# Performance work log

Measured on AMD Instinct MI355X. Metric: run time of the kernel, lower is better.

Reference implementation:

```python
import jax, jax.numpy as jnp
import numpy as np

# Mamba hyperparams (mamba_ssm defaults for d_model=128)
D_MODEL = 128
DEPTH = 8
D_INNER = 256   # expand=2
D_STATE = 16
D_CONV = 4
DT_RANK = 8     # ceil(D_MODEL/16)
EPS = 1e-5


def setup_inputs() -> dict:
    key = jax.random.key(0)
    ks = jax.random.split(key, 8)
    B, H, W = 1, 48, 48
    s = lambda k, shape, sc=0.02: jax.random.normal(k, shape, jnp.float32) * sc
    return {
        "x": jax.random.normal(ks[0], (B, D_MODEL, H, W), jnp.float32),
        "W_in": s(ks[1], (DEPTH, D_MODEL, 2 * D_INNER)),
        "conv_w": s(ks[2], (DEPTH, D_INNER, D_CONV), 0.2),
        "conv_b": jnp.zeros((DEPTH, D_INNER), jnp.float32),
        "W_xproj": s(ks[3], (DEPTH, D_INNER, DT_RANK + 2 * D_STATE)),
        "W_dt": s(ks[4], (DEPTH, DT_RANK, D_INNER), 0.1),
        "b_dt": jnp.full((DEPTH, D_INNER), -4.6, jnp.float32),  # softplus ~= 0.01
        "A_log": jnp.broadcast_to(
            jnp.log(jnp.arange(1, D_STATE + 1, dtype=jnp.float32)),
            (DEPTH, D_INNER, D_STATE)).copy(),
        "D_skip": jnp.ones((DEPTH, D_INNER), jnp.float32),
        "W_out": s(ks[5], (DEPTH, D_INNER, D_MODEL)),
        "rms_w": jnp.ones((DEPTH, D_MODEL), jnp.float32),
    }


def _rmsnorm(x, w):
    return x * jax.lax.rsqrt(jnp.mean(x * x, axis=-1, keepdims=True) + EPS) * w


def _mamba_layer(x, Wi, cw, cb, Wx, Wdt, bdt, Alog, Dp, Wo):
    # x: [B, L, D_MODEL]
    B, L, _ = x.shape
    xz = x @ Wi                                   # [B, L, 2*d_inner]
    xi, z = jnp.split(xz, 2, axis=-1)
    # causal depthwise conv1d, kernel D_CONV
    xp = jnp.pad(xi, ((0, 0), (D_CONV - 1, 0), (0, 0)))
    xc = sum(xp[:, k:k + L, :] * cw[:, k] for k in range(D_CONV)) + cb
    xc = jax.nn.silu(xc)                          # [B, L, d_inner]
    dbl = xc @ Wx                                 # [B, L, dt_rank + 2*d_state]
    dt_r = dbl[..., :DT_RANK]
    Bs = dbl[..., DT_RANK:DT_RANK + D_STATE]      # [B, L, d_state]
    Cs = dbl[..., DT_RANK + D_STATE:]
    dt = jax.nn.softplus(dt_r @ Wdt + bdt)        # [B, L, d_inner]
    A = -jnp.exp(Alog)                            # [d_inner, d_state]
    dA = jnp.exp(dt[..., None] * A)               # [B, L, d_inner, d_state]
    dBx = (dt * xc)[..., None] * Bs[:, :, None, :]
    # linear recurrence h_t = dA_t * h_{t-1} + dBx_t via parallel scan
    def comb(l, r):
        al, bl = l
        ar, br = r
        return ar * al, ar * bl + br
    _, h = jax.lax.associative_scan(comb, (dA, dBx), axis=1)
    y = jnp.einsum('blds,bls->bld', h, Cs) + Dp * xc
    y = y * jax.nn.silu(z)
    return y @ Wo                                 # [B, L, D_MODEL]


def reference(x, W_in, conv_w, conv_b, W_xproj, W_dt, b_dt, A_log, D_skip, W_out, rms_w):
    B, C, H, W = x.shape
    seq = x.reshape(B, C, H * W).transpose(0, 2, 1)  # [B, L, C]
    for l in range(DEPTH):
        seq = _mamba_layer(seq, W_in[l], conv_w[l], conv_b[l], W_xproj[l],
                           W_dt[l], b_dt[l], A_log[l], D_skip[l], W_out[l])
        seq = _rmsnorm(seq, rms_w[l])
    return seq.reshape(B, H, W, C).transpose(0, 3, 1, 2)
```

## Files before the change

kernel.cpp:

```cpp
#include <hip/hip_runtime.h>
#include <math.h>

#define LSEQ 2304
#define DM 128
#define DI 256
#define DS 16
#define RK 8
#define NCH 576
#define CLEN 4
#define NG 24
#define GS 24
#define NSI (DI*DS)
#define EPSF 1e-5f

__device__ __forceinline__ float silu_f(float s) { return s / (1.f + __expf(-s)); }
__device__ __forceinline__ float softplus_f(float x) { return (x > 20.f) ? x : log1pf(__expf(x)); }

template<bool FIRST>
__global__ __launch_bounds__(256, 4)
void k_in(const float* __restrict__ seq, const float* __restrict__ x0,
          const float* __restrict__ Wi,
          const float* __restrict__ cw, const float* __restrict__ cbias,
          float* __restrict__ xc_g, float* __restrict__ sz_g) {
    __shared__ float As[19 * 128];
    const int l0 = blockIdx.x * 16;
    const int half = blockIdx.y & 1;
    const bool isZ = blockIdx.y >= 2;
    const int tid = threadIdx.x;

    if (FIRST) {
        const int rlo = isZ ? 3 : 0;
        for (int idx = tid + rlo * 128; idx < 19 * 128; idx += 256) {
            const int r = idx >> 7, cc = idx & 127;
            const int l = l0 - 3 + r;
            As[idx] = (l >= 0) ? x0[cc * LSEQ + l] : 0.f;
        }
    } else if (!isZ) {
        for (int idx = tid; idx < 19 * 32; idx += 256) {
            const int r = idx >> 5, cq = (idx & 31) * 4;
            const int l = l0 - 3 + r;
            const float4 v = (l >= 0) ? *(const float4*)&seq[l * DM + cq]
                                      : make_float4(0.f, 0.f, 0.f, 0.f);
            *(float4*)&As[r * 128 + cq] = v;
        }
    } else {
        for (int idx = tid; idx < 16 * 32; idx += 256) {
            const int r = 3 + (idx >> 5), cq = (idx & 31) * 4;
            *(float4*)&As[r * 128 + cq] =
                *(const float4*)&seq[(l0 - 3 + r) * DM + cq];
        }
    }
    __syncthreads();

    const int c = tid & 127;
    const int rg = tid >> 7;
    const int d = half * 128 + c;

    if (!isZ) {
        float ax[11];
#pragma unroll
        for (int r = 0; r < 11; ++r) ax[r] = 0.f;
        for (int k4 = 0; k4 < 32; ++k4) {
            float bv[4];
#pragma unroll
            for (int u = 0; u < 4; ++u) bv[u] = Wi[(k4 * 4 + u) * 512 + d];
#pragma unroll
            for (int r = 0; r < 11; ++r) {
                const float4 a4 = *(const float4*)&As[(rg * 8 + r) * 128 + k4 * 4];
                ax[r] += a4.x * bv[0] + a4.y * bv[1] + a4.z * bv[2] + a4.w * bv[3];
            }
        }
        const float w0 = cw[d * 4 + 0], w1 = cw[d * 4 + 1];
        const float w2 = cw[d * 4 + 2], w3 = cw[d * 4 + 3];
        const float cbv = cbias[d];
#pragma unroll
        for (int rr = 0; rr < 8; ++rr) {
            const float v = silu_f(cbv + w0 * ax[rr] + w1 * ax[rr + 1] +
                                   w2 * ax[rr + 2] + w3 * ax[rr + 3]);
            xc_g[(l0 + rg * 8 + rr) * DI + d] = v;
        }
    } else {
        float az[8];
#pragma unroll
        for (int r = 0; r < 8; ++r) az[r] = 0.f;
        for (int k4 = 0; k4 < 32; ++k4) {
            float bv[4];
#pragma unroll
            for (int u = 0; u < 4; ++u) bv[u] = Wi[(k4 * 4 + u) * 512 + 256 + d];
#pragma unroll
            for (int r = 0; r < 8; ++r) {
                const float4 a4 = *(const float4*)&As[(rg * 8 + r + 3) * 128 + k4 * 4];
                az[r] += a4.x * bv[0] + a4.y * bv[1] + a4.z * bv[2] + a4.w * bv[3];
            }
        }
#pragma unroll
        for (int rr = 0; rr < 8; ++rr)
            sz_g[(l0 + rg * 8 + rr) * DI + d] = silu_f(az[rr]);
    }
}

__global__ __launch_bounds__(256, 4)
void k_mid2(const float* __restrict__ xc_g,
            const float* __restrict__ Wx,
            const float* __restrict__ Wdt, const float* __restrict__ bdt,
            const float* __restrict__ Alog,
            float* __restrict__ dbl_g, float* __restrict__ dt_g,
            float* __restrict__ P, float* __restrict__ S) {
    __shared__ float xcs[CLEN * 256];
    __shared__ float part[4 * 160];
    __shared__ float dtrs[CLEN * 8];
    __shared__ float dbls[CLEN * 32];
    const int c = blockIdx.x;
    const int l0 = c * CLEN;
    const int tid = threadIdx.x;
    const int d = tid;

    ((float4*)xcs)[tid] = ((const float4*)&xc_g[l0 * DI])[tid];
    __syncthreads();

    for (int task = tid; task < 640; task += 256) {
        const int kc = task / 160;
        const int o = task - kc * 160;
        const int r = o / 40, j = o - r * 40;
        const float* xr = &xcs[r * 256 + kc * 64];
        const float* wp = &Wx[(kc * 64) * 40 + j];
        float acc = 0.f;
#pragma unroll 8
        for (int k = 0; k < 64; ++k) acc += xr[k] * wp[k * 40];
        part[kc * 160 + o] = acc;
    }
    __syncthreads();
    if (tid < 160) {
        const float acc = part[tid] + part[160 + tid] + part[320 + tid] + part[480 + tid];
        const int r = tid / 40, j = tid - r * 40;
        if (j < RK) dtrs[r * 8 + j] = acc;
        else {
            dbls[r * 32 + (j - 8)] = acc;
            dbl_g[(l0 + r) * 32 + (j - 8)] = acc;
        }
    }
    __syncthreads();

    float dtv[CLEN], xcv[CLEN];
    {
        float wdt[8];
#pragma unroll
        for (int q = 0; q < 8; ++q) wdt[q] = Wdt[q * DI + d];
        const float bdv = bdt[d];
#pragma unroll
        for (int r = 0; r < CLEN; ++r) {
            float acc = bdv;
#pragma unroll
            for (int q = 0; q < 8; ++q) acc += dtrs[r * 8 + q] * wdt[q];
            dtv[r] = softplus_f(acc);
            dt_g[(l0 + r) * DI + d] = dtv[r];
            xcv[r] = xcs[r * 256 + d];
        }
    }

    float A[16], pr[16], hs[16];
#pragma unroll
    for (int v = 0; v < 4; ++v) {
        const float4 a4 = *(const float4*)&Alog[d * DS + v * 4];
        A[v * 4 + 0] = -__expf(a4.x);
        A[v * 4 + 1] = -__expf(a4.y);
        A[v * 4 + 2] = -__expf(a4.z);
        A[v * 4 + 3] = -__expf(a4.w);
    }
#pragma unroll
    for (int s = 0; s < 16; ++s) { pr[s] = 1.f; hs[s] = 0.f; }
#pragma unroll
    for (int t = 0; t < CLEN; ++t) {
        const float dtt = dtv[t];
        const float uv = dtt * xcv[t];
        const float* Brow = &dbls[t * 32];
#pragma unroll
        for (int s = 0; s < 16; ++s) {
            const float e = __expf(dtt * A[s]);
            pr[s] *= e;
            hs[s] = e * hs[s] + uv * Brow[s];
        }
    }
    const int base = c * NSI + d * DS;
#pragma unroll
    for (int v = 0; v < 4; ++v) {
        *(float4*)&P[base + v * 4] =
            make_float4(pr[v * 4], pr[v * 4 + 1], pr[v * 4 + 2], pr[v * 4 + 3]);
        *(float4*)&S[base + v * 4] =
            make_float4(hs[v * 4], hs[v * 4 + 1], hs[v * 4 + 2], hs[v * 4 + 3]);
    }
}

__global__ __launch_bounds__(256, 4)
void k_carry1(float* __restrict__ P, float* __restrict__ S,
              float* __restrict__ Pg, float* __restrict__ Sg) {
    const int g = blockIdx.x;
    const int i = blockIdx.y * 256 + threadIdx.x;
    float G = 0.f, Pp = 1.f;
    const int base = g * GS * NSI + i;
#pragma unroll 8
    for (int k = 0; k < GS; ++k) {
        const int idx = base + k * NSI;
        const float p = P[idx];
        const float s = S[idx];
        S[idx] = G;
        P[idx] = Pp;
        G = p * G + s;
        Pp *= p;
    }
    Pg[g * NSI + i] = Pp;
    Sg[g * NSI + i] = G;
}

__global__ __launch_bounds__(256, 4)
void k_carry2(const float* __restrict__ Pg, float* __restrict__ Sg) {
    const int i = blockIdx.x * 256 + threadIdx.x;
    float G = 0.f;
#pragma unroll 8
    for (int g = 0; g < NG; ++g) {
        const int idx = g * NSI + i;
        const float p = Pg[idx];
        const float s = Sg[idx];
        Sg[idx] = G;
        G = p * G + s;
    }
}

template<bool LAST>
__global__ __launch_bounds__(256, 3)
void k_tail(const float* __restrict__ dt_g, const float* __restrict__ xc_g,
            const float* __restrict__ dbl_g, const float* __restrict__ Alog,
            const float* __restrict__ Sloc, const float* __restrict__ Ppre,
            const float* __restrict__ Gc, const float* __restrict__ Dp,
            const float* __restrict__ sz_g, const float* __restrict__ Wo,
            const float* __restrict__ rmsw, float* __restrict__ seq,
            float* __restrict__ out) {
    __shared__ float dbls[CLEN * 32];
    __shared__ float Ys[CLEN * 256];
    __shared__ float partO[4 * CLEN * 128];
    __shared__ float Os[CLEN * 129];
    __shared__ float red[CLEN * 32];
    __shared__ float scaleS[CLEN];
    const int c = blockIdx.x;
    const int g = c / GS;
    const int l0 = c * CLEN;
    const int tid = threadIdx.x;
    const int d = tid;

    if (tid < CLEN * 32) dbls[tid] = dbl_g[l0 * 32 + tid];

    float A[16], h[16];
#pragma unroll
    for (int v = 0; v < 4; ++v) {
        const float4 a4 = *(const float4*)&Alog[d * DS + v * 4];
        A[v * 4 + 0] = -__expf(a4.x);
        A[v * 4 + 1] = -__expf(a4.y);
        A[v * 4 + 2] = -__expf(a4.z);
        A[v * 4 + 3] = -__expf(a4.w);
        const float4 s4 = *(const float4*)&Sloc[c * NSI + d * DS + v * 4];
        const float4 p4 = *(const float4*)&Ppre[c * NSI + d * DS + v * 4];
        const float4 g4 = *(const float4*)&Gc[g * NSI + d * DS + v * 4];
        h[v * 4 + 0] = s4.x + p4.x * g4.x;
        h[v * 4 + 1] = s4.y + p4.y * g4.y;
        h[v * 4 + 2] = s4.z + p4.z * g4.z;
        h[v * 4 + 3] = s4.w + p4.w * g4.w;
    }
    float dtv[CLEN], xcv[CLEN], szv[CLEN];
#pragma unroll
    for (int r = 0; r < CLEN; ++r) {
        dtv[r] = dt_g[(l0 + r) * DI + d];
        xcv[r] = xc_g[(l0 + r) * DI + d];
        szv[r] = sz_g[(l0 + r) * DI + d];
    }
    const float dskip = Dp[d];
    __syncthreads();
#pragma unroll
    for (int t = 0; t < CLEN; ++t) {
        const float dtt = dtv[t];
        const float uv = dtt * xcv[t];
        float sum = 0.f;
#pragma unroll
        for (int s = 0; s < 16; ++s) {
            const float e = __expf(dtt * A[s]);
            h[s] = e * h[s] + uv * dbls[t * 32 + s];
            sum += h[s] * dbls[t * 32 + 16 + s];
        }
        Ys[t * 256 + d] = (sum + dskip * xcv[t]) * szv[t];
    }
    __syncthreads();

    {
        const int ccp = tid & 63;
        const int kg = tid >> 6;
        float acc[CLEN][2];
#pragma unroll
        for (int r = 0; r < CLEN; ++r) { acc[r][0] = 0.f; acc[r][1] = 0.f; }
        const float* wp = &Wo[(kg * 64) * DM + ccp * 2];
        const float* yp = &Ys[kg * 64];
#pragma unroll 4
        for (int k4 = 0; k4 < 16; ++k4) {
            const float2 w0 = *(const float2*)(wp + (k4 * 4 + 0) * DM);
            const float2 w1 = *(const float2*)(wp + (k4 * 4 + 1) * DM);
            const float2 w2 = *(const float2*)(wp + (k4 * 4 + 2) * DM);
            const float2 w3 = *(const float2*)(wp + (k4 * 4 + 3) * DM);
            float4 y4[CLEN];
#pragma unroll
            for (int r = 0; r < CLEN; ++r)
                y4[r] = *(const float4*)&yp[r * 256 + k4 * 4];
#pragma unroll
            for (int r = 0; r < CLEN; ++r) {
                acc[r][0] += y4[r].x * w0.x; acc[r][1] += y4[r].x * w0.y;
            }
#pragma unroll
            for (int r = 0; r < CLEN; ++r) {
                acc[r][0] += y4[r].y * w1.x; acc[r][1] += y4[r].y * w1.y;
            }
#pragma unroll
            for (int r = 0; r < CLEN; ++r) {
                acc[r][0] += y4[r].z * w2.x; acc[r][1] += y4[r].z * w2.y;
            }
#pragma unroll
            for (int r = 0; r < CLEN; ++r) {
                acc[r][0] += y4[r].w * w3.x; acc[r][1] += y4[r].w * w3.y;
            }
        }
#pragma unroll
        for (int r = 0; r < CLEN; ++r) {
            partO[(kg * CLEN + r) * 128 + ccp * 2 + 0] = acc[r][0];
            partO[(kg * CLEN + r) * 128 + ccp * 2 + 1] = acc[r][1];
        }
        __syncthreads();
        for (int idx = tid; idx < CLEN * 128; idx += 256) {
            const int r = idx >> 7, cc = idx & 127;
            Os[r * 129 + cc] = partO[(0 * CLEN + r) * 128 + cc] +
                               partO[(1 * CLEN + r) * 128 + cc] +
                               partO[(2 * CLEN + r) * 128 + cc] +
                               partO[(3 * CLEN + r) * 128 + cc];
        }
        __syncthreads();
    }

    if (tid < CLEN * 32) {
        const int r = tid >> 5, part = tid & 31;
        float ss = 0.f;
#pragma unroll
        for (int i = 0; i < 4; ++i) {
            const float v = Os[r * 129 + part * 4 + i];
            ss += v * v;
        }
        red[tid] = ss;
    }
    __syncthreads();
    if (tid < CLEN) {
        float ss = 0.f;
#pragma unroll
        for (int p = 0; p < 32; ++p) ss += red[tid * 32 + p];
        scaleS[tid] = rsqrtf(ss * (1.f / DM) + EPSF);
    }
    __syncthreads();
    if (LAST) {
        for (int idx = tid; idx < CLEN * DM; idx += 256) {
            const int r = idx >> 7, cc = idx & 127;
            out[cc * LSEQ + (l0 + r)] = Os[r * 129 + cc] * scaleS[r] * rmsw[cc];
        }
    } else {
        for (int idx = tid; idx < CLEN * DM; idx += 256) {
            const int r = idx >> 7, cc = idx & 127;
            seq[(l0 + r) * DM + cc] = Os[r * 129 + cc] * scaleS[r] * rmsw[cc];
        }
    }
}

extern "C" void kernel_launch(void* const* d_in, const int* in_sizes, int n_in,
                              void* d_out, int out_size, void* d_ws, size_t ws_size,
                              hipStream_t stream) {
    const float* x    = (const float*)d_in[0];
    const float* W_in = (const float*)d_in[1];
    const float* cw   = (const float*)d_in[2];
    const float* cb   = (const float*)d_in[3];
    const float* Wx   = (const float*)d_in[4];
    const float* Wdt  = (const float*)d_in[5];
    const float* bdt  = (const float*)d_in[6];
    const float* Alog = (const float*)d_in[7];
    const float* Dp   = (const float*)d_in[8];
    const float* Wo   = (const float*)d_in[9];
    const float* rmsw = (const float*)d_in[10];
    float* out = (float*)d_out;

    float* ws   = (float*)d_ws;
    float* seq  = ws; ws += LSEQ * DM;
    float* szb  = ws; ws += LSEQ * DI;
    float* xcb  = ws; ws += LSEQ * DI;
    float* dtb  = ws; ws += LSEQ * DI;
    float* dblb = ws; ws += LSEQ * 32;
    float* Pb   = ws; ws += NCH * NSI;
    float* Sb   = ws; ws += NCH * NSI;
    float* Pgb  = ws; ws += NG * NSI;
    float* Sgb  = ws; ws += NG * NSI;

    for (int layer = 0; layer < 8; ++layer) {
        const float* Wi_l   = W_in + (size_t)layer * DM * 512;
        const float* cw_l   = cw   + (size_t)layer * DI * 4;
        const float* cb_l   = cb   + (size_t)layer * DI;
        const float* Wx_l   = Wx   + (size_t)layer * DI * 40;
        const float* Wdt_l  = Wdt  + (size_t)layer * RK * DI;
        const float* bdt_l  = bdt  + (size_t)layer * DI;
        const float* Alog_l = Alog + (size_t)layer * DI * DS;
        const float* Dp_l   = Dp   + (size_t)layer * DI;
        const float* Wo_l   = Wo   + (size_t)layer * DI * DM;
        const float* rmsw_l = rmsw + (size_t)layer * DM;

        if (layer == 0)
            k_in<true><<<dim3(144, 4), 256, 0, stream>>>(seq, x, Wi_l, cw_l, cb_l,
                                                         xcb, szb);
        else
            k_in<false><<<dim3(144, 4), 256, 0, stream>>>(seq, x, Wi_l, cw_l, cb_l,
                                                          xcb, szb);

        k_mid2<<<NCH, 256, 0, stream>>>(xcb, Wx_l, Wdt_l, bdt_l, Alog_l,
                                        dblb, dtb, Pb, Sb);

        k_carry1<<<dim3(NG, 16), 256, 0, stream>>>(Pb, Sb, Pgb, Sgb);
        k_carry2<<<16, 256, 0, stream>>>(Pgb, Sgb);

        if (layer == 7)
            k_tail<true><<<NCH, 256, 0, stream>>>(dtb, xcb, dblb, Alog_l, Sb, Pb,
                                                  Sgb, Dp_l, szb, Wo_l, rmsw_l,
                                                  seq, out);
        else
            k_tail<false><<<NCH, 256, 0, stream>>>(dtb, xcb, dblb, Alog_l, Sb, Pb,
                                                   Sgb, Dp_l, szb, Wo_l, rmsw_l,
                                                   seq, out);
    }
}
```

Before: 556.7 us.

## Double threads per block in k_in, k_mid2 and k_tail, splitting state dimension

```diff
diff --git a/kernel.cpp b/kernel.cpp
--- a/kernel.cpp
+++ b/kernel.cpp
@@ -17,7 +17,7 @@
 __device__ __forceinline__ float softplus_f(float x) { return (x > 20.f) ? x : log1pf(__expf(x)); }
 
 template<bool FIRST>
-__global__ __launch_bounds__(256, 4)
+__global__ __launch_bounds__(512, 4)
 void k_in(const float* __restrict__ seq, const float* __restrict__ x0,
           const float* __restrict__ Wi,
           const float* __restrict__ cw, const float* __restrict__ cbias,
@@ -30,13 +30,13 @@
 
     if (FIRST) {
         const int rlo = isZ ? 3 : 0;
-        for (int idx = tid + rlo * 128; idx < 19 * 128; idx += 256) {
+        for (int idx = tid + rlo * 128; idx < 19 * 128; idx += 512) {
             const int r = idx >> 7, cc = idx & 127;
             const int l = l0 - 3 + r;
             As[idx] = (l >= 0) ? x0[cc * LSEQ + l] : 0.f;
         }
     } else if (!isZ) {
-        for (int idx = tid; idx < 19 * 32; idx += 256) {
+        for (int idx = tid; idx < 19 * 32; idx += 512) {
             const int r = idx >> 5, cq = (idx & 31) * 4;
             const int l = l0 - 3 + r;
             const float4 v = (l >= 0) ? *(const float4*)&seq[l * DM + cq]
@@ -44,7 +44,7 @@
             *(float4*)&As[r * 128 + cq] = v;
         }
     } else {
-        for (int idx = tid; idx < 16 * 32; idx += 256) {
+        for (int idx = tid; idx < 16 * 32; idx += 512) {
             const int r = 3 + (idx >> 5), cq = (idx & 31) * 4;
             *(float4*)&As[r * 128 + cq] =
                 *(const float4*)&seq[(l0 - 3 + r) * DM + cq];
@@ -57,16 +57,16 @@
     const int d = half * 128 + c;
 
     if (!isZ) {
-        float ax[11];
-#pragma unroll
-        for (int r = 0; r < 11; ++r) ax[r] = 0.f;
+        float ax[7];
+#pragma unroll
+        for (int r = 0; r < 7; ++r) ax[r] = 0.f;
         for (int k4 = 0; k4 < 32; ++k4) {
             float bv[4];
 #pragma unroll
             for (int u = 0; u < 4; ++u) bv[u] = Wi[(k4 * 4 + u) * 512 + d];
 #pragma unroll
-            for (int r = 0; r < 11; ++r) {
-                const float4 a4 = *(const float4*)&As[(rg * 8 + r) * 128 + k4 * 4];
+            for (int r = 0; r < 7; ++r) {
+                const float4 a4 = *(const float4*)&As[(rg * 4 + r) * 128 + k4 * 4];
                 ax[r] += a4.x * bv[0] + a4.y * bv[1] + a4.z * bv[2] + a4.w * bv[3];
             }
         }
@@ -74,32 +74,32 @@
         const float w2 = cw[d * 4 + 2], w3 = cw[d * 4 + 3];
         const float cbv = cbias[d];
 #pragma unroll
-        for (int rr = 0; rr < 8; ++rr) {
+        for (int rr = 0; rr < 4; ++rr) {
             const float v = silu_f(cbv + w0 * ax[rr] + w1 * ax[rr + 1] +
                                    w2 * ax[rr + 2] + w3 * ax[rr + 3]);
-            xc_g[(l0 + rg * 8 + rr) * DI + d] = v;
+            xc_g[(l0 + rg * 4 + rr) * DI + d] = v;
         }
     } else {
-        float az[8];
-#pragma unroll
-        for (int r = 0; r < 8; ++r) az[r] = 0.f;
+        float az[4];
+#pragma unroll
+        for (int r = 0; r < 4; ++r) az[r] = 0.f;
         for (int k4 = 0; k4 < 32; ++k4) {
             float bv[4];
 #pragma unroll
             for (int u = 0; u < 4; ++u) bv[u] = Wi[(k4 * 4 + u) * 512 + 256 + d];
 #pragma unroll
-            for (int r = 0; r < 8; ++r) {
-                const float4 a4 = *(const float4*)&As[(rg * 8 + r + 3) * 128 + k4 * 4];
+            for (int r = 0; r < 4; ++r) {
+                const float4 a4 = *(const float4*)&As[(rg * 4 + r + 3) * 128 + k4 * 4];
                 az[r] += a4.x * bv[0] + a4.y * bv[1] + a4.z * bv[2] + a4.w * bv[3];
             }
         }
 #pragma unroll
-        for (int rr = 0; rr < 8; ++rr)
-            sz_g[(l0 + rg * 8 + rr) * DI + d] = silu_f(az[rr]);
-    }
-}
-
-__global__ __launch_bounds__(256, 4)
+        for (int rr = 0; rr < 4; ++rr)
+            sz_g[(l0 + rg * 4 + rr) * DI + d] = silu_f(az[rr]);
+    }
+}
+
+__global__ __launch_bounds__(512, 4)
 void k_mid2(const float* __restrict__ xc_g,
             const float* __restrict__ Wx,
             const float* __restrict__ Wdt, const float* __restrict__ bdt,
@@ -113,12 +113,13 @@
     const int c = blockIdx.x;
     const int l0 = c * CLEN;
     const int tid = threadIdx.x;
-    const int d = tid;
-
-    ((float4*)xcs)[tid] = ((const float4*)&xc_g[l0 * DI])[tid];
-    __syncthreads();
-
-    for (int task = tid; task < 640; task += 256) {
+    const int d = tid >> 1;
+    const int sh = tid & 1;
+
+    if (tid < 256) ((float4*)xcs)[tid] = ((const float4*)&xc_g[l0 * DI])[tid];
+    __syncthreads();
+
+    for (int task = tid; task < 640; task += 512) {
         const int kc = task / 160;
         const int o = task - kc * 160;
         const int r = o / 40, j = o - r * 40;
@@ -153,37 +154,37 @@
 #pragma unroll
             for (int q = 0; q < 8; ++q) acc += dtrs[r * 8 + q] * wdt[q];
             dtv[r] = softplus_f(acc);
-            dt_g[(l0 + r) * DI + d] = dtv[r];
+            if (sh == 0) dt_g[(l0 + r) * DI + d] = dtv[r];
             xcv[r] = xcs[r * 256 + d];
         }
     }
 
-    float A[16], pr[16], hs[16];
-#pragma unroll
-    for (int v = 0; v < 4; ++v) {
-        const float4 a4 = *(const float4*)&Alog[d * DS + v * 4];
+    float A[8], pr[8], hs[8];
+#pragma unroll
+    for (int v = 0; v < 2; ++v) {
+        const float4 a4 = *(const float4*)&Alog[tid * 8 + v * 4];
         A[v * 4 + 0] = -__expf(a4.x);
         A[v * 4 + 1] = -__expf(a4.y);
         A[v * 4 + 2] = -__expf(a4.z);
         A[v * 4 + 3] = -__expf(a4.w);
     }
 #pragma unroll
-    for (int s = 0; s < 16; ++s) { pr[s] = 1.f; hs[s] = 0.f; }
+    for (int s = 0; s < 8; ++s) { pr[s] = 1.f; hs[s] = 0.f; }
 #pragma unroll
     for (int t = 0; t < CLEN; ++t) {
         const float dtt = dtv[t];
         const float uv = dtt * xcv[t];
-        const float* Brow = &dbls[t * 32];
-#pragma unroll
-        for (int s = 0; s < 16; ++s) {
+        const float* Brow = &dbls[t * 32 + sh * 8];
+#pragma unroll
+        for (int s = 0; s < 8; ++s) {
             const float e = __expf(dtt * A[s]);
             pr[s] *= e;
             hs[s] = e * hs[s] + uv * Brow[s];
         }
     }
-    const int base = c * NSI + d * DS;
-#pragma unroll
-    for (int v = 0; v < 4; ++v) {
+    const int base = c * NSI + tid * 8;
+#pragma unroll
+    for (int v = 0; v < 2; ++v) {
         *(float4*)&P[base + v * 4] =
             make_float4(pr[v * 4], pr[v * 4 + 1], pr[v * 4 + 2], pr[v * 4 + 3]);
         *(float4*)&S[base + v * 4] =
@@ -227,7 +228,7 @@
 }
 
 template<bool LAST>
-__global__ __launch_bounds__(256, 3)
+__global__ __launch_bounds__(512, 4)
 void k_tail(const float* __restrict__ dt_g, const float* __restrict__ xc_g,
             const float* __restrict__ dbl_g, const float* __restrict__ Alog,
             const float* __restrict__ Sloc, const float* __restrict__ Ppre,
@@ -237,7 +238,7 @@
             float* __restrict__ out) {
     __shared__ float dbls[CLEN * 32];
     __shared__ float Ys[CLEN * 256];
-    __shared__ float partO[4 * CLEN * 128];
+    __shared__ float partO[8 * CLEN * 128];
     __shared__ float Os[CLEN * 129];
     __shared__ float red[CLEN * 32];
     __shared__ float scaleS[CLEN];
@@ -245,21 +246,22 @@
     const int g = c / GS;
     const int l0 = c * CLEN;
     const int tid = threadIdx.x;
-    const int d = tid;
+    const int d = tid >> 1;
+    const int sh = tid & 1;
 
     if (tid < CLEN * 32) dbls[tid] = dbl_g[l0 * 32 + tid];
 
-    float A[16], h[16];
-#pragma unroll
-    for (int v = 0; v < 4; ++v) {
-        const float4 a4 = *(const float4*)&Alog[d * DS + v * 4];
+    float A[8], h[8];
+#pragma unroll
+    for (int v = 0; v < 2; ++v) {
+        const float4 a4 = *(const float4*)&Alog[tid * 8 + v * 4];
         A[v * 4 + 0] = -__expf(a4.x);
         A[v * 4 + 1] = -__expf(a4.y);
         A[v * 4 + 2] = -__expf(a4.z);
         A[v * 4 + 3] = -__expf(a4.w);
-        const float4 s4 = *(const float4*)&Sloc[c * NSI + d * DS + v * 4];
-        const float4 p4 = *(const float4*)&Ppre[c * NSI + d * DS + v * 4];
-        const float4 g4 = *(const float4*)&Gc[g * NSI + d * DS + v * 4];
+        const float4 s4 = *(const float4*)&Sloc[c * NSI + tid * 8 + v * 4];
+        const float4 p4 = *(const float4*)&Ppre[c * NSI + tid * 8 + v * 4];
+        const float4 g4 = *(const float4*)&Gc[g * NSI + tid * 8 + v * 4];
         h[v * 4 + 0] = s4.x + p4.x * g4.x;
         h[v * 4 + 1] = s4.y + p4.y * g4.y;
         h[v * 4 + 2] = s4.z + p4.z * g4.z;
@@ -278,14 +280,17 @@
     for (int t = 0; t < CLEN; ++t) {
         const float dtt = dtv[t];
         const float uv = dtt * xcv[t];
-        float sum = 0.f;
-#pragma unroll
-        for (int s = 0; s < 16; ++s) {
+        const float* Brow = &dbls[t * 32 + sh * 8];
+        const float* Crow = &dbls[t * 32 + 16 + sh * 8];
+        float ps = 0.f;
+#pragma unroll
+        for (int s = 0; s < 8; ++s) {
             const float e = __expf(dtt * A[s]);
-            h[s] = e * h[s] + uv * dbls[t * 32 + s];
-            sum += h[s] * dbls[t * 32 + 16 + s];
-        }
-        Ys[t * 256 + d] = (sum + dskip * xcv[t]) * szv[t];
+            h[s] = e * h[s] + uv * Brow[s];
+            ps += h[s] * Crow[s];
+        }
+        ps += __shfl_xor(ps, 1);
+        if (sh == 0) Ys[t * 256 + d] = (ps + dskip * xcv[t]) * szv[t];
     }
     __syncthreads();
 
@@ -295,10 +300,10 @@
         float acc[CLEN][2];
 #pragma unroll
         for (int r = 0; r < CLEN; ++r) { acc[r][0] = 0.f; acc[r][1] = 0.f; }
-        const float* wp = &Wo[(kg * 64) * DM + ccp * 2];
-        const float* yp = &Ys[kg * 64];
+        const float* wp = &Wo[(kg * 32) * DM + ccp * 2];
+        const float* yp = &Ys[kg * 32];
 #pragma unroll 4
-        for (int k4 = 0; k4 < 16; ++k4) {
+        for (int k4 = 0; k4 < 8; ++k4) {
             const float2 w0 = *(const float2*)(wp + (k4 * 4 + 0) * DM);
             const float2 w1 = *(const float2*)(wp + (k4 * 4 + 1) * DM);
             const float2 w2 = *(const float2*)(wp + (k4 * 4 + 2) * DM);
@@ -330,22 +335,23 @@
             partO[(kg * CLEN + r) * 128 + ccp * 2 + 1] = acc[r][1];
         }
         __syncthreads();
-        for (int idx = tid; idx < CLEN * 128; idx += 256) {
+        for (int idx = tid; idx < CLEN * 128; idx += 512) {
             const int r = idx >> 7, cc = idx & 127;
-            Os[r * 129 + cc] = partO[(0 * CLEN + r) * 128 + cc] +
-                               partO[(1 * CLEN + r) * 128 + cc] +
-                               partO[(2 * CLEN + r) * 128 + cc] +
-                               partO[(3 * CLEN + r) * 128 + cc];
+            float s = 0.f;
+#pragma unroll
+            for (int kgi = 0; kgi < 8; ++kgi)
+                s += partO[(kgi * CLEN + r) * 128 + cc];
+            Os[r * 129 + cc] = s;
         }
         __syncthreads();
     }
 
     if (tid < CLEN * 32) {
-        const int r = tid >> 5, part = tid & 31;
+        const int r = tid >> 5, pp = tid & 31;
         float ss = 0.f;
 #pragma unroll
         for (int i = 0; i < 4; ++i) {
-            const float v = Os[r * 129 + part * 4 + i];
+            const float v = Os[r * 129 + pp * 4 + i];
             ss += v * v;
         }
         red[tid] = ss;
@@ -359,12 +365,12 @@
     }
     __syncthreads();
     if (LAST) {
-        for (int idx = tid; idx < CLEN * DM; idx += 256) {
+        for (int idx = tid; idx < CLEN * DM; idx += 512) {
             const int r = idx >> 7, cc = idx & 127;
             out[cc * LSEQ + (l0 + r)] = Os[r * 129 + cc] * scaleS[r] * rmsw[cc];
         }
     } else {
-        for (int idx = tid; idx < CLEN * DM; idx += 256) {
+        for (int idx = tid; idx < CLEN * DM; idx += 512) {
             const int r = idx >> 7, cc = idx & 127;
             seq[(l0 + r) * DM + cc] = Os[r * 129 + cc] * scaleS[r] * rmsw[cc];
         }
@@ -411,24 +417,24 @@
         const float* rmsw_l = rmsw + (size_t)layer * DM;
 
         if (layer == 0)
-            k_in<true><<<dim3(144, 4), 256, 0, stream>>>(seq, x, Wi_l, cw_l, cb_l,
+            k_in<true><<<dim3(144, 4), 512, 0, stream>>>(seq, x, Wi_l, cw_l, cb_l,
                                                          xcb, szb);
         else
-            k_in<false><<<dim3(144, 4), 256, 0, stream>>>(seq, x, Wi_l, cw_l, cb_l,
+            k_in<false><<<dim3(144, 4), 512, 0, stream>>>(seq, x, Wi_l, cw_l, cb_l,
                                                           xcb, szb);
 
-        k_mid2<<<NCH, 256, 0, stream>>>(xcb, Wx_l, Wdt_l, bdt_l, Alog_l,
+        k_mid2<<<NCH, 512, 0, stream>>>(xcb, Wx_l, Wdt_l, bdt_l, Alog_l,
                                         dblb, dtb, Pb, Sb);
 
         k_carry1<<<dim3(NG, 16), 256, 0, stream>>>(Pb, Sb, Pgb, Sgb);
         k_carry2<<<16, 256, 0, stream>>>(Pgb, Sgb);
 
         if (layer == 7)
-            k_tail<true><<<NCH, 256, 0, stream>>>(dtb, xcb, dblb, Alog_l, Sb, Pb,
+            k_tail<true><<<NCH, 512, 0, stream>>>(dtb, xcb, dblb, Alog_l, Sb, Pb,
                                                   Sgb, Dp_l, szb, Wo_l, rmsw_l,
                                                   seq, out);
         else
-            k_tail<false><<<NCH, 256, 0, stream>>>(dtb, xcb, dblb, Alog_l, Sb, Pb,
+            k_tail<false><<<NCH, 512, 0, stream>>>(dtb, xcb, dblb, Alog_l, Sb, Pb,
                                                    Sgb, Dp_l, szb, Wo_l, rmsw_l,
                                                    seq, out);
     }
```

New measurement: 543.9 us (median of 2 runs). 1.02x faster.
